# Kernel optimization log

Measured on AMD Instinct MI355X. Metric: run time of the kernel, lower is better.

Reference implementation:

```python
import jax, jax.numpy as jnp
import numpy as np

NUM_EMBEDDINGS = 1024
EMBEDDING_DIM = 256
COMMITMENT_COST = 0.25
DECAY = 0.99
EPSILON = 1e-05


def setup_inputs() -> dict:
    key = jax.random.key(0)
    k1, k2, k3 = jax.random.split(key, 3)
    z_e = jax.random.normal(k1, (32, 32, 32, EMBEDDING_DIM), dtype=jnp.float32)
    embedding = jax.random.normal(k2, (NUM_EMBEDDINGS, EMBEDDING_DIM), dtype=jnp.float32)
    ema_cluster_size = jnp.zeros((NUM_EMBEDDINGS,), dtype=jnp.float32)
    ema_w = jax.random.normal(k3, (NUM_EMBEDDINGS, EMBEDDING_DIM), dtype=jnp.float32)
    return {"z_e": z_e, "embedding": embedding,
            "ema_cluster_size": ema_cluster_size, "ema_w": ema_w}


def reference(z_e, embedding, ema_cluster_size, ema_w):
    K, D = embedding.shape
    flat = z_e.reshape(-1, D)  # [N, D]
    distances = (jnp.sum(flat * flat, axis=1, keepdims=True)
                 - 2.0 * (flat @ embedding.T)
                 + jnp.sum(embedding * embedding, axis=1))
    encoding_indices = jnp.argmin(distances, axis=1)  # [N]
    # one_hot @ embedding == gather of nearest codes
    z_q = embedding[encoding_indices].reshape(z_e.shape)

    # EMA codebook update (training branch, torch no_grad)
    counts = jax.ops.segment_sum(jnp.ones_like(encoding_indices, dtype=flat.dtype),
                                 encoding_indices, num_segments=K)  # encodings.sum(0)
    dw = jax.ops.segment_sum(flat, encoding_indices, num_segments=K)  # encodings.T @ flat
    new_cluster_size = DECAY * ema_cluster_size + (1.0 - DECAY) * counts
    new_ema_w = DECAY * ema_w + (1.0 - DECAY) * dw
    n = jnp.sum(new_cluster_size)
    cluster_size = (new_cluster_size + EPSILON) / (n + K * EPSILON) * n
    new_embedding = new_ema_w / cluster_size[:, None]

    codebook_loss = jnp.mean((z_q - jax.lax.stop_gradient(z_e)) ** 2)
    commitment_loss = COMMITMENT_COST * jnp.mean((z_e - jax.lax.stop_gradient(z_q)) ** 2)
    vq_loss = codebook_loss + commitment_loss
    z_q_st = z_e + jax.lax.stop_gradient(z_q - z_e)  # straight-through
    return (z_q_st, vq_loss, encoding_indices,
            new_embedding, new_cluster_size, new_ema_w)
```

## Files before the change

kernel.cpp:

```cpp
#include <hip/hip_runtime.h>

#define DECAY_F 0.99f
#define OMD_F   0.01f
#define EPS_F   1e-5f

typedef __attribute__((ext_vector_type(8)))  __bf16 bf16x8;
typedef __attribute__((ext_vector_type(16))) float  f32x16;

#define WSB_CNTI     0
#define WSB_LOSS     4096
#define WSB_DWACC    8192
#define WSB_CSUM     1056768
#define WSB_ENORM    1056832
#define WSB_IDX      1060928
#define WSB_EHI      1192000
#define WSB_ELO      1716288
#define WSB_SORT     2240576
#define WSB_CURS     2371648

#define OUT_ZQ    0
#define OUT_LOSS  8388608
#define OUT_IDX   8388609
#define OUT_EMB   8421377
#define OUT_CS    8683521
#define OUT_EMAW  8684545

__device__ __forceinline__ unsigned short f2bf(float x) {
    unsigned u = __builtin_bit_cast(unsigned, x);
    u += 0x7fffu + ((u >> 16) & 1u);
    return (unsigned short)(u >> 16);
}
__device__ __forceinline__ float bf2f(unsigned short h) {
    return __builtin_bit_cast(float, (unsigned)h << 16);
}
__device__ __forceinline__ void split8(const float4 a, const float4 b,
                                       uint4& hi, uint4& lo) {
    float f[8] = {a.x, a.y, a.z, a.w, b.x, b.y, b.z, b.w};
    unsigned short h[8], l[8];
    #pragma unroll
    for (int i = 0; i < 8; ++i) {
        h[i] = f2bf(f[i]);
        l[i] = f2bf(f[i] - bf2f(h[i]));
    }
    hi.x = (unsigned)h[0] | ((unsigned)h[1] << 16);
    hi.y = (unsigned)h[2] | ((unsigned)h[3] << 16);
    hi.z = (unsigned)h[4] | ((unsigned)h[5] << 16);
    hi.w = (unsigned)h[6] | ((unsigned)h[7] << 16);
    lo.x = (unsigned)l[0] | ((unsigned)l[1] << 16);
    lo.y = (unsigned)l[2] | ((unsigned)l[3] << 16);
    lo.z = (unsigned)l[4] | ((unsigned)l[5] << 16);
    lo.w = (unsigned)l[6] | ((unsigned)l[7] << 16);
}

__global__ __launch_bounds__(256)
void esplit_enorm_kernel(const float* __restrict__ emb,
                         unsigned short* __restrict__ e_hi,
                         unsigned short* __restrict__ e_lo,
                         float* __restrict__ enorm,
                         float* __restrict__ dwacc,
                         int* __restrict__ cnt,
                         float* __restrict__ lossbuf,
                         int* __restrict__ cursor) {
    const int tid = threadIdx.x, lane = tid & 63, wv = tid >> 6;
    const int gthread = blockIdx.x * 256 + tid;

    *(float4*)(dwacc + (size_t)gthread * 4) = make_float4(0.f, 0.f, 0.f, 0.f);
    if (gthread < 1024) { cnt[gthread] = 0; cursor[gthread] = 0; }
    if (gthread < 256)  lossbuf[gthread] = 0.f;

    if (gthread < 32768) {
        const int F     = gthread;
        const int chunk = F >> 6;
        const int lh6   = (F >> 5) & 1;
        const int l31f  = F & 31;
        const int g     = chunk >> 4;
        const int kc    = (chunk >> 1) & 7;
        const int kk    = chunk & 1;
        const int k     = g * 32 + l31f;
        const int d0    = kc * 32 + (kk * 2 + lh6) * 8;
        const float4 v0 = *(const float4*)(emb + (size_t)k * 256 + d0);
        const float4 v1 = *(const float4*)(emb + (size_t)k * 256 + d0 + 4);
        uint4 h, l;
        split8(v0, v1, h, l);
        *(uint4*)((char*)e_hi + (size_t)F * 16) = h;
        *(uint4*)((char*)e_lo + (size_t)F * 16) = l;
    }

    const int k = blockIdx.x * 4 + wv;
    const float4 v = *(const float4*)(emb + (size_t)k * 256 + lane * 4);
    float s = v.x * v.x + v.y * v.y + v.z * v.z + v.w * v.w;
    #pragma unroll
    for (int off = 32; off > 0; off >>= 1) s += __shfl_down(s, off);
    if (lane == 0) enorm[k] = s;
}

__global__ __launch_bounds__(256, 2)
void argmin_kernel(const float* __restrict__ z,
                   const unsigned short* __restrict__ e_hi,
                   const unsigned short* __restrict__ e_lo,
                   const float* __restrict__ enorm,
                   const float* __restrict__ emb,
                   int* __restrict__ idx, float* __restrict__ idxf,
                   float* __restrict__ out_zq, int* __restrict__ cnt) {
    __shared__ unsigned short Ah[32 * 512], Al[32 * 512];

    const int tid  = threadIdx.x;
    const int lane = tid & 63;
    const int wv   = tid >> 6;
    const int l31  = lane & 31, lh = lane >> 5;
    const int row0 = blockIdx.x * 64;
    const int vOff = lane * 16;

    #pragma unroll
    for (int c8 = 0; c8 < 8; ++c8) {
        const int C  = wv * 8 + c8;
        const int i  = C >> 4, kc = (C >> 1) & 7, kk = C & 1;
        const int row = row0 + i * 32 + l31;
        const int d0  = kc * 32 + (kk * 2 + lh) * 8;
        const float4 v0 = *(const float4*)(z + (size_t)row * 256 + d0);
        const float4 v1 = *(const float4*)(z + (size_t)row * 256 + d0 + 4);
        uint4 h, l;
        split8(v0, v1, h, l);
        *(uint4*)((char*)Ah + (size_t)C * 1024 + vOff) = h;
        *(uint4*)((char*)Al + (size_t)C * 1024 + vOff) = l;
    }
    __syncthreads();

    f32x16 acc[2][2];
    #pragma unroll
    for (int i = 0; i < 2; ++i)
        #pragma unroll
        for (int j = 0; j < 2; ++j) acc[i][j] = (f32x16)0.0f;

    float bestd[2][16];
    int   besti[2][16];
    #pragma unroll
    for (int i = 0; i < 2; ++i)
        #pragma unroll
        for (int r = 0; r < 16; ++r) { bestd[i][r] = 3.4e38f; besti[i][r] = 0; }

    const char* ehW = (const char*)e_hi + (size_t)wv * 32768;
    const char* elW = (const char*)e_lo + (size_t)wv * 32768;
    uint4 b0h[4], b0l[4], b1h[4], b1l[4];
    auto loadB = [&](int s, uint4* bh, uint4* bl) {
        const int off = ((s >> 3) << 17) + ((s & 7) << 11);
        const char* ph = ehW + off;
        const char* pl = elW + off;
        bh[0] = *(const uint4*)(ph + vOff);
        bh[1] = *(const uint4*)(ph + vOff + 1024);
        bh[2] = *(const uint4*)(ph + vOff + 16384);
        bh[3] = *(const uint4*)(ph + vOff + 17408);
        bl[0] = *(const uint4*)(pl + vOff);
        bl[1] = *(const uint4*)(pl + vOff + 1024);
        bl[2] = *(const uint4*)(pl + vOff + 16384);
        bl[3] = *(const uint4*)(pl + vOff + 17408);
    };
    auto compute = [&](int s, const uint4* bh4, const uint4* bl4) {
        const int kcoff = (s & 7) << 11;
        const char* pa = (const char*)Ah + vOff + kcoff;
        const char* pb = (const char*)Al + vOff + kcoff;
        #pragma unroll
        for (int kk = 0; kk < 2; ++kk) {
            bf16x8 bh[2], bl[2];
            #pragma unroll
            for (int j = 0; j < 2; ++j) {
                bh[j] = __builtin_bit_cast(bf16x8, bh4[j * 2 + kk]);
                bl[j] = __builtin_bit_cast(bf16x8, bl4[j * 2 + kk]);
            }
            #pragma unroll
            for (int i = 0; i < 2; ++i) {
                const bf16x8 ah = __builtin_bit_cast(bf16x8,
                    *(const uint4*)(pa + i * 16384 + kk * 1024));
                const bf16x8 al = __builtin_bit_cast(bf16x8,
                    *(const uint4*)(pb + i * 16384 + kk * 1024));
                #pragma unroll
                for (int j = 0; j < 2; ++j) {
                    acc[i][j] = __builtin_amdgcn_mfma_f32_32x32x16_bf16(ah, bh[j], acc[i][j], 0, 0, 0);
                    acc[i][j] = __builtin_amdgcn_mfma_f32_32x32x16_bf16(al, bh[j], acc[i][j], 0, 0, 0);
                    acc[i][j] = __builtin_amdgcn_mfma_f32_32x32x16_bf16(ah, bl[j], acc[i][j], 0, 0, 0);
                }
            }
        }
        if ((s & 7) == 7) {
            const int csp = s >> 3;
            #pragma unroll
            for (int j = 0; j < 2; ++j) {
                const int col = csp * 256 + wv * 64 + j * 32 + l31;
                const float en = enorm[col];
                #pragma unroll
                for (int i = 0; i < 2; ++i)
                    #pragma unroll
                    for (int r = 0; r < 16; ++r) {
                        const float d = fmaf(-2.0f, acc[i][j][r], en);
                        if (d < bestd[i][r]) { bestd[i][r] = d; besti[i][r] = col; }
                    }
            }
            #pragma unroll
            for (int i = 0; i < 2; ++i)
                #pragma unroll
                for (int j = 0; j < 2; ++j) acc[i][j] = (f32x16)0.0f;
        }
    };

    loadB(0, b0h, b0l);
    for (int s = 0; s < 32; s += 2) {
        loadB(s + 1, b1h, b1l);
        compute(s, b0h, b0l);
        if (s + 2 < 32) loadB(s + 2, b0h, b0l);
        compute(s + 1, b1h, b1l);
    }

    #pragma unroll
    for (int m = 1; m < 32; m <<= 1) {
        #pragma unroll
        for (int i = 0; i < 2; ++i)
            #pragma unroll
            for (int r = 0; r < 16; ++r) {
                const float od = __shfl_xor(bestd[i][r], m);
                const int   oi = __shfl_xor(besti[i][r], m);
                if (od < bestd[i][r] || (od == bestd[i][r] && oi < besti[i][r])) {
                    bestd[i][r] = od; besti[i][r] = oi;
                }
            }
    }

    __syncthreads();
    float* mg_d = (float*)Ah;
    int*   mg_i = (int*)Ah + 256;
    if (l31 == 0) {
        #pragma unroll
        for (int i = 0; i < 2; ++i)
            #pragma unroll
            for (int r = 0; r < 16; ++r) {
                const int rloc = i * 32 + (r & 3) + 8 * (r >> 2) + 4 * lh;
                mg_d[wv * 64 + rloc] = bestd[i][r];
                mg_i[wv * 64 + rloc] = besti[i][r];
            }
    }
    __syncthreads();
    if (tid < 64) {
        float d0 = mg_d[tid];
        int   i0 = mg_i[tid];
        #pragma unroll
        for (int w = 1; w < 4; ++w) {
            const float dw = mg_d[w * 64 + tid];
            const int   iw = mg_i[w * 64 + tid];
            if (dw < d0 || (dw == d0 && iw < i0)) { d0 = dw; i0 = iw; }
        }
        const int n = row0 + tid;
        idx[n] = i0; idxf[n] = (float)i0;
        atomicAdd(&cnt[i0], 1);
        mg_i[tid] = i0;
    }
    __syncthreads();

    #pragma unroll 4
    for (int r = 0; r < 16; ++r) {
        const int row = wv * 16 + r;
        const int code = mg_i[row];
        const float4 e4 = *(const float4*)(emb + (size_t)code * 256 + lane * 4);
        *(float4*)(out_zq + (size_t)(row0 + row) * 256 + lane * 4) = e4;
    }
}

__global__ __launch_bounds__(256)
void scatter_kernel(const int* __restrict__ idx, const int* __restrict__ cnt,
                    int* __restrict__ cursor, int* __restrict__ sorted) {
    __shared__ int sbase[1024];
    __shared__ int wsum[4];
    const int t = threadIdx.x, lane = t & 63, wv = t >> 6;

    int c[4]; int ts = 0;
    #pragma unroll
    for (int i = 0; i < 4; ++i) { c[i] = cnt[t * 4 + i]; ts += c[i]; }
    int v = ts;
    #pragma unroll
    for (int o = 1; o < 64; o <<= 1) { const int u = __shfl_up(v, o); if (lane >= o) v += u; }
    if (lane == 63) wsum[wv] = v;
    __syncthreads();
    int wbase = 0;
    #pragma unroll
    for (int w = 0; w < 4; ++w) if (w < wv) wbase += wsum[w];
    int base = wbase + v - ts;
    #pragma unroll
    for (int i = 0; i < 4; ++i) { sbase[t * 4 + i] = base; base += c[i]; }
    __syncthreads();

    const int n = blockIdx.x * 256 + t;
    const int k = idx[n];
    const int r = atomicAdd(&cursor[k], 1);
    sorted[sbase[k] + r] = n;
}

__global__ __launch_bounds__(256)
void dw_kernel(const float* __restrict__ z, const float* __restrict__ emb,
               const float* __restrict__ enorm,
               const int* __restrict__ sorted, const int* __restrict__ idx,
               float* __restrict__ dwacc, float* __restrict__ lossbuf) {
    const int lane = threadIdx.x & 63;
    const int w    = blockIdx.x * 4 + (threadIdx.x >> 6);
    const int r0   = w * 16;
    const int srow = sorted[r0 + (lane & 15)];
    const int skey = idx[srow];

    float4 s = make_float4(0.f, 0.f, 0.f, 0.f);
    float sumsq = 0.f;
    int cntr = 0;
    int krun = __shfl(skey, 0);

    auto flush = [&](int k) {
        const float4 e = *(const float4*)(emb + (size_t)k * 256 + lane * 4);
        float val = sumsq - 2.0f * (e.x * s.x + e.y * s.y + e.z * s.z + e.w * s.w);
        #pragma unroll
        for (int off = 32; off > 0; off >>= 1) val += __shfl_down(val, off);
        if (lane == 0) atomicAdd(&lossbuf[k & 255], val + (float)cntr * enorm[k]);
        float* p = dwacc + (size_t)k * 256 + lane * 4;
        atomicAdd(p + 0, s.x); atomicAdd(p + 1, s.y);
        atomicAdd(p + 2, s.z); atomicAdd(p + 3, s.w);
    };

    #pragma unroll 8
    for (int j = 0; j < 16; ++j) {
        const int row = __shfl(srow, j);
        const int k   = __shfl(skey, j);
        if (k != krun) {
            flush(krun);
            s = make_float4(0.f, 0.f, 0.f, 0.f);
            sumsq = 0.f; cntr = 0; krun = k;
        }
        const float4 v = *(const float4*)(z + (size_t)row * 256 + lane * 4);
        s.x += v.x; s.y += v.y; s.z += v.z; s.w += v.w;
        sumsq += v.x * v.x + v.y * v.y + v.z * v.z + v.w * v.w;
        ++cntr;
    }
    flush(krun);
}

__global__ __launch_bounds__(256)
void update_w_kernel(const float* __restrict__ ema_cs, const int* __restrict__ cnt,
                     const float* __restrict__ ema_w, const float* __restrict__ dwacc,
                     const float* __restrict__ lossbuf,
                     float* __restrict__ out_cs,
                     float* __restrict__ out_emb, float* __restrict__ out_emaw,
                     float* __restrict__ out_loss) {
    __shared__ float red[256];
    const int t = threadIdx.x;

    float fv[4]; float fsum = 0.f;
    #pragma unroll
    for (int i = 0; i < 4; ++i) {
        const int k4 = t * 4 + i;
        const float f = DECAY_F * ema_cs[k4] + OMD_F * (float)cnt[k4];
        fv[i] = f; fsum += f;
    }
    red[t] = fsum; __syncthreads();
    #pragma unroll
    for (int off = 128; off > 0; off >>= 1) {
        if (t < off) red[t] += red[t + off];
        __syncthreads();
    }
    const float n_total = red[0];
    __syncthreads();

    if (blockIdx.x == 0) {
        #pragma unroll
        for (int i = 0; i < 4; ++i) out_cs[t * 4 + i] = fv[i];
        red[t] = lossbuf[t]; __syncthreads();
        #pragma unroll
        for (int off = 128; off > 0; off >>= 1) {
            if (t < off) red[t] += red[t + off];
            __syncthreads();
        }
        if (t == 0) out_loss[0] = 1.25f * red[0] / 8388608.0f;
    }

    const int g = blockIdx.x * 256 + t;
    const int k = g >> 6;
    const float fk = DECAY_F * ema_cs[k] + OMD_F * (float)cnt[k];
    const float cs = (fk + EPS_F) / (n_total + 1024.0f * EPS_F) * n_total;

    const float4 w4 = *(const float4*)(ema_w + (size_t)g * 4);
    const float4 d4 = *(const float4*)(dwacc + (size_t)g * 4);
    float4 nw, ne;
    nw.x = DECAY_F * w4.x + OMD_F * d4.x;
    nw.y = DECAY_F * w4.y + OMD_F * d4.y;
    nw.z = DECAY_F * w4.z + OMD_F * d4.z;
    nw.w = DECAY_F * w4.w + OMD_F * d4.w;
    ne.x = nw.x / cs; ne.y = nw.y / cs; ne.z = nw.z / cs; ne.w = nw.w / cs;
    *(float4*)(out_emaw + (size_t)g * 4) = nw;
    *(float4*)(out_emb  + (size_t)g * 4) = ne;
}

extern "C" void kernel_launch(void* const* d_in, const int* in_sizes, int n_in,
                              void* d_out, int out_size, void* d_ws, size_t ws_size,
                              hipStream_t stream) {
    const float* z      = (const float*)d_in[0];
    const float* emb    = (const float*)d_in[1];
    const float* ema_cs = (const float*)d_in[2];
    const float* ema_w  = (const float*)d_in[3];

    float* out = (float*)d_out;
    char*  wsb = (char*)d_ws;

    int*            cnt     = (int*)(wsb + WSB_CNTI);
    float*          lossbuf = (float*)(wsb + WSB_LOSS);
    float*          dwacc   = (float*)(wsb + WSB_DWACC);
    float*          enorm   = (float*)(wsb + WSB_ENORM);
    int*            idx     = (int*)(wsb + WSB_IDX);
    unsigned short* e_hi    = (unsigned short*)(wsb + WSB_EHI);
    unsigned short* e_lo    = (unsigned short*)(wsb + WSB_ELO);
    int*            sorted  = (int*)(wsb + WSB_SORT);
    int*            cursor  = (int*)(wsb + WSB_CURS);

    float* out_zq   = out + OUT_ZQ;
    float* out_loss = out + OUT_LOSS;
    float* out_idxf = out + OUT_IDX;
    float* out_emb  = out + OUT_EMB;
    float* out_cs   = out + OUT_CS;
    float* out_emaw = out + OUT_EMAW;

    esplit_enorm_kernel<<<256, 256, 0, stream>>>(emb, e_hi, e_lo, enorm,
                                                 dwacc, cnt, lossbuf, cursor);
    argmin_kernel<<<512, 256, 0, stream>>>(z, e_hi, e_lo, enorm, emb,
                                           idx, out_idxf, out_zq, cnt);
    scatter_kernel<<<128, 256, 0, stream>>>(idx, cnt, cursor, sorted);
    dw_kernel<<<512, 256, 0, stream>>>(z, emb, enorm, sorted, idx, dwacc, lossbuf);
    update_w_kernel<<<256, 256, 0, stream>>>(ema_cs, cnt, ema_w, dwacc, lossbuf,
                                             out_cs, out_emb, out_emaw, out_loss);
}
```

Baseline: 200.6 us.

## Halve argmin row tile to 32 rows per block and raise occupancy

Each argmin block now handles 32 rows instead of 64, with one MFMA row tile per wave. The grid doubles, LDS per block is halved, and launch bounds allow three blocks per CU. The aim is more resident waves and better balance across CUs. The cost is that every codebook fragment loaded from global memory feeds half as many MFMAs, so codebook read traffic doubles.

```diff
diff --git a/kernel.cpp b/kernel.cpp
--- a/kernel.cpp
+++ b/kernel.cpp
@@ -94,7 +94,7 @@
     if (lane == 0) enorm[k] = s;
 }
 
-__global__ __launch_bounds__(256, 2)
+__global__ __launch_bounds__(256, 3)
 void argmin_kernel(const float* __restrict__ z,
                    const unsigned short* __restrict__ e_hi,
                    const unsigned short* __restrict__ e_lo,
@@ -102,20 +102,20 @@
                    const float* __restrict__ emb,
                    int* __restrict__ idx, float* __restrict__ idxf,
                    float* __restrict__ out_zq, int* __restrict__ cnt) {
-    __shared__ unsigned short Ah[32 * 512], Al[32 * 512];
+    __shared__ unsigned short Ah[16 * 512], Al[16 * 512];
 
     const int tid  = threadIdx.x;
     const int lane = tid & 63;
     const int wv   = tid >> 6;
     const int l31  = lane & 31, lh = lane >> 5;
-    const int row0 = blockIdx.x * 64;
+    const int row0 = blockIdx.x * 32;
     const int vOff = lane * 16;
 
     #pragma unroll
-    for (int c8 = 0; c8 < 8; ++c8) {
-        const int C  = wv * 8 + c8;
-        const int i  = C >> 4, kc = (C >> 1) & 7, kk = C & 1;
-        const int row = row0 + i * 32 + l31;
+    for (int c8 = 0; c8 < 4; ++c8) {
+        const int C  = wv * 4 + c8;
+        const int kc = C >> 1, kk = C & 1;
+        const int row = row0 + l31;
         const int d0  = kc * 32 + (kk * 2 + lh) * 8;
         const float4 v0 = *(const float4*)(z + (size_t)row * 256 + d0);
         const float4 v1 = *(const float4*)(z + (size_t)row * 256 + d0 + 4);
@@ -126,18 +126,14 @@
     }
     __syncthreads();
 
-    f32x16 acc[2][2];
-    #pragma unroll
-    for (int i = 0; i < 2; ++i)
-        #pragma unroll
-        for (int j = 0; j < 2; ++j) acc[i][j] = (f32x16)0.0f;
-
-    float bestd[2][16];
-    int   besti[2][16];
-    #pragma unroll
-    for (int i = 0; i < 2; ++i)
-        #pragma unroll
-        for (int r = 0; r < 16; ++r) { bestd[i][r] = 3.4e38f; besti[i][r] = 0; }
+    f32x16 acc[2];
+    #pragma unroll
+    for (int j = 0; j < 2; ++j) acc[j] = (f32x16)0.0f;
+
+    float bestd[16];
+    int   besti[16];
+    #pragma unroll
+    for (int r = 0; r < 16; ++r) { bestd[r] = 3.4e38f; besti[r] = 0; }
 
     const char* ehW = (const char*)e_hi + (size_t)wv * 32768;
     const char* elW = (const char*)e_lo + (size_t)wv * 32768;
@@ -167,18 +163,15 @@
                 bh[j] = __builtin_bit_cast(bf16x8, bh4[j * 2 + kk]);
                 bl[j] = __builtin_bit_cast(bf16x8, bl4[j * 2 + kk]);
             }
+            const bf16x8 ah = __builtin_bit_cast(bf16x8,
+                *(const uint4*)(pa + kk * 1024));
+            const bf16x8 al = __builtin_bit_cast(bf16x8,
+                *(const uint4*)(pb + kk * 1024));
             #pragma unroll
-            for (int i = 0; i < 2; ++i) {
-                const bf16x8 ah = __builtin_bit_cast(bf16x8,
-                    *(const uint4*)(pa + i * 16384 + kk * 1024));
-                const bf16x8 al = __builtin_bit_cast(bf16x8,
-                    *(const uint4*)(pb + i * 16384 + kk * 1024));
-                #pragma unroll
-                for (int j = 0; j < 2; ++j) {
-                    acc[i][j] = __builtin_amdgcn_mfma_f32_32x32x16_bf16(ah, bh[j], acc[i][j], 0, 0, 0);
-                    acc[i][j] = __builtin_amdgcn_mfma_f32_32x32x16_bf16(al, bh[j], acc[i][j], 0, 0, 0);
-                    acc[i][j] = __builtin_amdgcn_mfma_f32_32x32x16_bf16(ah, bl[j], acc[i][j], 0, 0, 0);
-                }
+            for (int j = 0; j < 2; ++j) {
+                acc[j] = __builtin_amdgcn_mfma_f32_32x32x16_bf16(ah, bh[j], acc[j], 0, 0, 0);
+                acc[j] = __builtin_amdgcn_mfma_f32_32x32x16_bf16(al, bh[j], acc[j], 0, 0, 0);
+                acc[j] = __builtin_amdgcn_mfma_f32_32x32x16_bf16(ah, bl[j], acc[j], 0, 0, 0);
             }
         }
         if ((s & 7) == 7) {
@@ -188,17 +181,13 @@
                 const int col = csp * 256 + wv * 64 + j * 32 + l31;
                 const float en = enorm[col];
                 #pragma unroll
-                for (int i = 0; i < 2; ++i)
-                    #pragma unroll
-                    for (int r = 0; r < 16; ++r) {
-                        const float d = fmaf(-2.0f, acc[i][j][r], en);
-                        if (d < bestd[i][r]) { bestd[i][r] = d; besti[i][r] = col; }
-                    }
+                for (int r = 0; r < 16; ++r) {
+                    const float d = fmaf(-2.0f, acc[j][r], en);
+                    if (d < bestd[r]) { bestd[r] = d; besti[r] = col; }
+                }
             }
             #pragma unroll
-            for (int i = 0; i < 2; ++i)
-                #pragma unroll
-                for (int j = 0; j < 2; ++j) acc[i][j] = (f32x16)0.0f;
+            for (int j = 0; j < 2; ++j) acc[j] = (f32x16)0.0f;
         }
     };
 
@@ -213,38 +202,34 @@
     #pragma unroll
     for (int m = 1; m < 32; m <<= 1) {
         #pragma unroll
-        for (int i = 0; i < 2; ++i)
-            #pragma unroll
-            for (int r = 0; r < 16; ++r) {
-                const float od = __shfl_xor(bestd[i][r], m);
-                const int   oi = __shfl_xor(besti[i][r], m);
-                if (od < bestd[i][r] || (od == bestd[i][r] && oi < besti[i][r])) {
-                    bestd[i][r] = od; besti[i][r] = oi;
-                }
+        for (int r = 0; r < 16; ++r) {
+            const float od = __shfl_xor(bestd[r], m);
+            const int   oi = __shfl_xor(besti[r], m);
+            if (od < bestd[r] || (od == bestd[r] && oi < besti[r])) {
+                bestd[r] = od; besti[r] = oi;
             }
+        }
     }
 
     __syncthreads();
     float* mg_d = (float*)Ah;
-    int*   mg_i = (int*)Ah + 256;
+    int*   mg_i = (int*)Ah + 128;
     if (l31 == 0) {
         #pragma unroll
-        for (int i = 0; i < 2; ++i)
-            #pragma unroll
-            for (int r = 0; r < 16; ++r) {
-                const int rloc = i * 32 + (r & 3) + 8 * (r >> 2) + 4 * lh;
-                mg_d[wv * 64 + rloc] = bestd[i][r];
-                mg_i[wv * 64 + rloc] = besti[i][r];
-            }
-    }
-    __syncthreads();
-    if (tid < 64) {
+        for (int r = 0; r < 16; ++r) {
+            const int rloc = (r & 3) + 8 * (r >> 2) + 4 * lh;
+            mg_d[wv * 32 + rloc] = bestd[r];
+            mg_i[wv * 32 + rloc] = besti[r];
+        }
+    }
+    __syncthreads();
+    if (tid < 32) {
         float d0 = mg_d[tid];
         int   i0 = mg_i[tid];
         #pragma unroll
         for (int w = 1; w < 4; ++w) {
-            const float dw = mg_d[w * 64 + tid];
-            const int   iw = mg_i[w * 64 + tid];
+            const float dw = mg_d[w * 32 + tid];
+            const int   iw = mg_i[w * 32 + tid];
             if (dw < d0 || (dw == d0 && iw < i0)) { d0 = dw; i0 = iw; }
         }
         const int n = row0 + tid;
@@ -255,8 +240,8 @@
     __syncthreads();
 
     #pragma unroll 4
-    for (int r = 0; r < 16; ++r) {
-        const int row = wv * 16 + r;
+    for (int r = 0; r < 8; ++r) {
+        const int row = wv * 8 + r;
         const int code = mg_i[row];
         const float4 e4 = *(const float4*)(emb + (size_t)code * 256 + lane * 4);
         *(float4*)(out_zq + (size_t)(row0 + row) * 256 + lane * 4) = e4;
@@ -421,8 +406,8 @@
 
     esplit_enorm_kernel<<<256, 256, 0, stream>>>(emb, e_hi, e_lo, enorm,
                                                  dwacc, cnt, lossbuf, cursor);
-    argmin_kernel<<<512, 256, 0, stream>>>(z, e_hi, e_lo, enorm, emb,
-                                           idx, out_idxf, out_zq, cnt);
+    argmin_kernel<<<1024, 256, 0, stream>>>(z, e_hi, e_lo, enorm, emb,
+                                            idx, out_idxf, out_zq, cnt);
     scatter_kernel<<<128, 256, 0, stream>>>(idx, cnt, cursor, sorted);
     dw_kernel<<<512, 256, 0, stream>>>(z, emb, enorm, sorted, idx, dwacc, lossbuf);
     update_w_kernel<<<256, 256, 0, stream>>>(ema_cs, cnt, ema_w, dwacc, lossbuf,
```

Result: slower. 476.5 us (+137.5%).
